# Performance work log

Measured on AMD Instinct MI355X. Metric: run time of the kernel, lower is better.

Reference implementation:

```python
import jax, jax.numpy as jnp
import numpy as np

N_NODES = 16384
N_EDGES = 524288
N_GRAPHS = 256
IN_CH = 128
H_CH = 128   # per-head channels
HEADS = 2
LAYER_DIM = HEADS * H_CH  # 256, concat=True
POOL_DIM = 3 * LAYER_DIM  # 768
OUT_CH = 1
NEG_SLOPE = 0.2


def setup_inputs() -> dict:
    key = jax.random.key(0)
    ks = jax.random.split(key, 20)
    s = lambda k, shape, fan: jax.random.normal(k, shape, jnp.float32) * (1.0 / np.sqrt(fan))
    inp = {
        "x": jax.random.normal(ks[0], (N_NODES, IN_CH), jnp.float32),
        "edge_index": jax.random.randint(ks[1], (2, N_EDGES), 0, N_NODES, jnp.int64),
        "batch": jnp.sort(jax.random.randint(ks[2], (N_NODES,), 0, N_GRAPHS, jnp.int64)),
        # GATv2 layer 1 (in=128)
        "Wl1": s(ks[3], (IN_CH, LAYER_DIM), IN_CH), "Wr1": s(ks[4], (IN_CH, LAYER_DIM), IN_CH),
        "att1": s(ks[5], (HEADS, H_CH), H_CH), "b1": jnp.zeros((LAYER_DIM,), jnp.float32),
        # GATv2 layer 2 (in=256)
        "Wl2": s(ks[6], (LAYER_DIM, LAYER_DIM), LAYER_DIM), "Wr2": s(ks[7], (LAYER_DIM, LAYER_DIM), LAYER_DIM),
        "att2": s(ks[8], (HEADS, H_CH), H_CH), "b2": jnp.zeros((LAYER_DIM,), jnp.float32),
        # GATv2 layer 3 (in=256)
        "Wl3": s(ks[9], (LAYER_DIM, LAYER_DIM), LAYER_DIM), "Wr3": s(ks[10], (LAYER_DIM, LAYER_DIM), LAYER_DIM),
        "att3": s(ks[11], (HEADS, H_CH), H_CH), "b3": jnp.zeros((LAYER_DIM,), jnp.float32),
        # FFN (dropout inactive at eval)
        "fW1": s(ks[12], (POOL_DIM, POOL_DIM), POOL_DIM), "fb1": jnp.zeros((POOL_DIM,), jnp.float32),
        "fW2": s(ks[13], (POOL_DIM, OUT_CH), POOL_DIM), "fb2": jnp.zeros((OUT_CH,), jnp.float32),
    }
    return inp


def _gatv2(x, src, dst, Wl, Wr, att, b):
    """PyG GATv2Conv: per-edge score a . LeakyReLU(Wl x_src + Wr x_dst),
    softmax over incoming edges per destination, weighted scatter-add of Wl x_src."""
    n = x.shape[0]
    xl = (x @ Wl).reshape(n, HEADS, H_CH)  # source messages
    xr = (x @ Wr).reshape(n, HEADS, H_CH)  # target query
    e = jax.nn.leaky_relu(xl[src] + xr[dst], NEG_SLOPE)          # [E,H,C]
    logits = jnp.einsum('ehc,hc->eh', e, att)                    # [E,H]
    m = jax.ops.segment_max(logits, dst, num_segments=n)         # per-dst max (self-loops guarantee nonempty)
    ev = jnp.exp(logits - m[dst])
    denom = jax.ops.segment_sum(ev, dst, num_segments=n)
    alpha = ev / denom[dst]                                       # [E,H]
    out = jax.ops.segment_sum(alpha[..., None] * xl[src], dst, num_segments=n)  # [N,H,C]
    return out.reshape(n, LAYER_DIM) + b


def reference(x, edge_index, batch, Wl1, Wr1, att1, b1, Wl2, Wr2, att2, b2,
              Wl3, Wr3, att3, b3, fW1, fb1, fW2, fb2):
    n = x.shape[0]
    loops = jnp.arange(n, dtype=edge_index.dtype)
    src = jnp.concatenate([edge_index[0], loops])  # add_self_loops=True default
    dst = jnp.concatenate([edge_index[1], loops])
    h1 = _gatv2(x, src, dst, Wl1, Wr1, att1, b1)
    h2 = _gatv2(h1, src, dst, Wl2, Wr2, att2, b2)
    h3 = _gatv2(h2, src, dst, Wl3, Wr3, att3, b3)
    pool = lambda h: jax.ops.segment_sum(h, batch, num_segments=N_GRAPHS)
    h = jnp.concatenate([pool(h1), pool(h2), pool(h3)], axis=1)   # [G,768]
    h = jax.nn.relu(h @ fW1 + fb1)
    return h @ fW2 + fb2                                           # [G,1]
```

## Files before the change

### kernel.cpp

```cpp
#include <hip/hip_runtime.h>

#define NNODES 16384
#define NEDGES 524288
#define NETOT  (NEDGES + NNODES)
#define NGRAPH 256

typedef __attribute__((ext_vector_type(8))) short short8;
typedef __attribute__((ext_vector_type(4))) float f32x4;
typedef __attribute__((ext_vector_type(2))) float f32x2;
typedef __attribute__((ext_vector_type(4))) unsigned int u32x4;

__device__ __forceinline__ float b2f(unsigned short u){
  union { unsigned int i; float f; } v; v.i = ((unsigned int)u) << 16; return v.f;
}
__device__ __forceinline__ unsigned short f2b(float f){
  union { float f; unsigned int i; } v; v.f = f;
  unsigned int r = v.i + 0x7FFFu + ((v.i >> 16) & 1u);
  return (unsigned short)(r >> 16);
}
__device__ __forceinline__ f32x2 unpack2(unsigned int u){
  union { unsigned int i; float f; } lo, hi;
  lo.i = u << 16; hi.i = u & 0xFFFF0000u;
  f32x2 r; r[0] = lo.f; r[1] = hi.f; return r;
}

__global__ void __launch_bounds__(256) zero_deg(int* __restrict__ deg){
  deg[blockIdx.x * 256 + threadIdx.x] = 0;
}

__global__ void __launch_bounds__(256) count_deg(const int* __restrict__ ei, int* __restrict__ deg){
  int i = blockIdx.x * 256 + threadIdx.x;
  int d = (i < NEDGES) ? ei[NEDGES + i] : (i - NEDGES);
  atomicAdd(&deg[d], 1);
}

__global__ void __launch_bounds__(256) scan1(const int* __restrict__ deg,
                                             int* __restrict__ incl, int* __restrict__ bsum){
  __shared__ int ws[4];
  const int b = blockIdx.x, t = threadIdx.x, lane = t & 63, w = t >> 6;
  int v = deg[b * 256 + t];
  int x = v;
  #pragma unroll
  for(int o = 1; o < 64; o <<= 1){ int u = __shfl_up(x, o, 64); if(lane >= o) x += u; }
  if(lane == 63) ws[w] = x;
  __syncthreads();
  int add = 0;
  #pragma unroll
  for(int j = 0; j < 4; j++) if(j < w) add += ws[j];
  incl[b * 256 + t] = x + add;
  if(t == 255) bsum[b] = x + add;
}

__global__ void __launch_bounds__(256) scan3(const int* __restrict__ deg, const int* __restrict__ incl,
                                             const int* __restrict__ bsum,
                                             int* __restrict__ row_off, int* __restrict__ cursor){
  __shared__ int boff_s;
  const int b = blockIdx.x, t = threadIdx.x;
  if(t < 64){
    int v = (t < b) ? bsum[t] : 0;
    #pragma unroll
    for(int o = 32; o > 0; o >>= 1) v += __shfl_xor(v, o, 64);
    if(t == 0) boff_s = v;
  }
  __syncthreads();
  const int i = b * 256 + t;
  int inc = incl[i] + boff_s;
  row_off[i + 1] = inc;
  cursor[i] = inc - deg[i];
  if(i == 0) row_off[0] = 0;
}

__global__ void __launch_bounds__(256) fill_csr(const int* __restrict__ ei, int* __restrict__ cursor,
                                                int* __restrict__ col_src){
  int i = blockIdx.x * 256 + threadIdx.x;
  int s, d;
  if(i < NEDGES){ s = ei[i]; d = ei[NEDGES + i]; }
  else          { s = i - NEDGES; d = s; }
  int p = atomicAdd(&cursor[d], 1);
  col_src[p] = s;
}

__global__ void __launch_bounds__(256) prep(const float* __restrict__ x,
                                            const float* __restrict__ Wl1, const float* __restrict__ Wr1,
                                            const float* __restrict__ Wl2, const float* __restrict__ Wr2,
                                            const float* __restrict__ Wl3, const float* __restrict__ Wr3,
                                            unsigned short* __restrict__ xb,
                                            unsigned short* __restrict__ Wt1,
                                            unsigned short* __restrict__ Wt2,
                                            unsigned short* __restrict__ Wt3){
  const int b = blockIdx.x, t = threadIdx.x;
  if(b < 8192){
    int i = b * 256 + t;
    xb[i] = f2b(x[i]);
    return;
  }
  const float *Wl, *Wr; unsigned short* Wt; int K, i;
  if(b < 8192 + 256){ Wl = Wl1; Wr = Wr1; Wt = Wt1; K = 128; i = (b - 8192) * 256 + t; }
  else if(b < 8192 + 256 + 512){ Wl = Wl2; Wr = Wr2; Wt = Wt2; K = 256; i = (b - 8448) * 256 + t; }
  else { Wl = Wl3; Wr = Wr3; Wt = Wt3; K = 256; i = (b - 8960) * 256 + t; }
  int k = i >> 9, c = i & 511;
  float val = (c < 256) ? Wl[(size_t)k * 256 + c] : Wr[(size_t)k * 256 + (c - 256)];
  Wt[(size_t)c * K + k] = f2b(val);
}

template<int K>
__global__ void __launch_bounds__(256) gemm_xw(const unsigned short* __restrict__ A,
                                               const unsigned short* __restrict__ Wt,
                                               unsigned short* __restrict__ Cout){
  __shared__ unsigned short As[64][40];
  __shared__ unsigned short Bs[128][40];
  const int t = threadIdx.x;
  const int rowbase = blockIdx.x * 64;
  const int colbase = blockIdx.y * 128;
  const int wave = t >> 6, lane = t & 63;
  const int lrow = lane & 15, kg = lane >> 4;

  f32x4 acc[8] = {};

  for(int kt = 0; kt < K; kt += 32){
    {
      int oct = t & 3, r = t >> 2;
      *(short8*)(&As[r][oct * 8]) =
        *(const short8*)(A + (size_t)(rowbase + r) * K + kt + oct * 8);
    }
    {
      int n = t & 127, kh = (t >> 7) * 16;
      const unsigned short* gw = Wt + (size_t)(colbase + n) * K + kt + kh;
      short8 v0 = *(const short8*)gw;
      short8 v1 = *(const short8*)(gw + 8);
      *(short8*)(&Bs[n][kh])     = v0;
      *(short8*)(&Bs[n][kh + 8]) = v1;
    }
    __syncthreads();
    short8 afrag = *(const short8*)(&As[wave * 16 + lrow][kg * 8]);
    #pragma unroll
    for(int fc = 0; fc < 8; fc++){
      short8 bfrag = *(const short8*)(&Bs[fc * 16 + lrow][kg * 8]);
      acc[fc] = __builtin_amdgcn_mfma_f32_16x16x32_bf16(afrag, bfrag, acc[fc], 0, 0, 0);
    }
    __syncthreads();
  }
  #pragma unroll
  for(int fc = 0; fc < 8; fc++)
    #pragma unroll
    for(int r = 0; r < 4; r++){
      int row = rowbase + wave * 16 + kg * 4 + r;
      int col = colbase + fc * 16 + lrow;
      Cout[(size_t)row * 512 + col] = f2b(acc[fc][r]);
    }
}

__global__ void __launch_bounds__(256) edge_agg(const unsigned short* __restrict__ xlb,
                                                const int* __restrict__ row_off,
                                                const int* __restrict__ col_src,
                                                const float* __restrict__ att,
                                                const float* __restrict__ bias,
                                                unsigned short* __restrict__ hout){
  const int n = (blockIdx.x * 256 + threadIdx.x) >> 6;
  const int lane = threadIdx.x & 63;
  const int eg = lane >> 4;
  const int c0 = (lane & 15) * 16;
  f32x2 xr[8], at[8];
  {
    const unsigned short* xp = xlb + (size_t)n * 512 + 256 + c0;
    u32x4 v0 = *(const u32x4*)xp;
    u32x4 v1 = *(const u32x4*)(xp + 8);
    xr[0] = unpack2(v0.x); xr[1] = unpack2(v0.y); xr[2] = unpack2(v0.z); xr[3] = unpack2(v0.w);
    xr[4] = unpack2(v1.x); xr[5] = unpack2(v1.y); xr[6] = unpack2(v1.z); xr[7] = unpack2(v1.w);
    #pragma unroll
    for(int i = 0; i < 8; i++) at[i] = *(const f32x2*)(att + c0 + 2 * i);
  }
  float s = 0.f;
  f32x2 ac[8] = {};
  const int beg = row_off[n], end = row_off[n + 1];
  for(int ch = beg; ch < end; ch += 64){
    int idx = ch + lane;
    int si = (idx < end) ? col_src[idx] : 0;
    int cnt = end - ch; if(cnt > 64) cnt = 64;
    int src0 = __shfl(si, eg);
    const unsigned short* gp0 = xlb + (size_t)src0 * 512 + c0;
    u32x4 va = *(const u32x4*)gp0;
    u32x4 vb = *(const u32x4*)(gp0 + 8);
    for(int k = 0; k < cnt; k += 4){
      int nk = k + 4 + eg; nk = (nk > 63) ? 63 : nk;
      int nsrc = __shfl(si, nk);
      const unsigned short* gpn = xlb + (size_t)nsrc * 512 + c0;
      u32x4 na = *(const u32x4*)gpn;
      u32x4 nb = *(const u32x4*)(gpn + 8);
      f32x2 x0 = unpack2(va.x), x1 = unpack2(va.y), x2 = unpack2(va.z), x3 = unpack2(va.w);
      f32x2 x4 = unpack2(vb.x), x5 = unpack2(vb.y), x6 = unpack2(vb.z), x7 = unpack2(vb.w);
      f32x2 e, p2;
      e = x0 + xr[0]; e = __builtin_elementwise_max(e, e * 0.2f); p2  = e * at[0];
      e = x1 + xr[1]; e = __builtin_elementwise_max(e, e * 0.2f); p2 += e * at[1];
      e = x2 + xr[2]; e = __builtin_elementwise_max(e, e * 0.2f); p2 += e * at[2];
      e = x3 + xr[3]; e = __builtin_elementwise_max(e, e * 0.2f); p2 += e * at[3];
      e = x4 + xr[4]; e = __builtin_elementwise_max(e, e * 0.2f); p2 += e * at[4];
      e = x5 + xr[5]; e = __builtin_elementwise_max(e, e * 0.2f); p2 += e * at[5];
      e = x6 + xr[6]; e = __builtin_elementwise_max(e, e * 0.2f); p2 += e * at[6];
      e = x7 + xr[7]; e = __builtin_elementwise_max(e, e * 0.2f); p2 += e * at[7];
      float p = p2[0] + p2[1];
      p += __shfl_xor(p, 1); p += __shfl_xor(p, 2); p += __shfl_xor(p, 4);
      float pe = (k + eg < cnt) ? __expf(p) : 0.f;
      s += pe;
      f32x2 pe2 = {pe, pe};
      ac[0] += pe2 * x0; ac[1] += pe2 * x1; ac[2] += pe2 * x2; ac[3] += pe2 * x3;
      ac[4] += pe2 * x4; ac[5] += pe2 * x5; ac[6] += pe2 * x6; ac[7] += pe2 * x7;
      va = na; vb = nb;
    }
  }
  s += __shfl_xor(s, 16); s += __shfl_xor(s, 32);
  #pragma unroll
  for(int i = 0; i < 8; i++){
    ac[i][0] += __shfl_xor(ac[i][0], 16); ac[i][0] += __shfl_xor(ac[i][0], 32);
    ac[i][1] += __shfl_xor(ac[i][1], 16); ac[i][1] += __shfl_xor(ac[i][1], 32);
  }
  if(eg == 0){
    float inv = 1.f / s;
    unsigned short o[16];
    #pragma unroll
    for(int i = 0; i < 8; i++){
      o[2 * i]     = f2b(fmaf(ac[i][0], inv, bias[c0 + 2 * i]));
      o[2 * i + 1] = f2b(fmaf(ac[i][1], inv, bias[c0 + 2 * i + 1]));
    }
    unsigned short* hp = hout + (size_t)n * 256 + c0;
    *(u32x4*)hp       = *(const u32x4*)&o[0];
    *(u32x4*)(hp + 8) = *(const u32x4*)&o[8];
  }
}

__device__ __forceinline__ int lbound(const int* __restrict__ a, int n, int v){
  int lo = 0, hi = n;
  while(lo < hi){ int mid = (lo + hi) >> 1; if(a[mid] < v) lo = mid + 1; else hi = mid; }
  return lo;
}

__global__ void __launch_bounds__(256) pool_accum(const unsigned short* __restrict__ h,
                                                  const int* __restrict__ batch,
                                                  float* __restrict__ pool, int slot){
  __shared__ float red[8][264];
  const int g = blockIdx.x, t = threadIdx.x;
  const int ng = t >> 5, c0 = (t & 31) * 8;
  const int lo = lbound(batch, NNODES, g);
  const int hi = lbound(batch, NNODES, g + 1);
  f32x2 a0 = {0.f,0.f}, a1 = {0.f,0.f}, a2 = {0.f,0.f}, a3 = {0.f,0.f};
  for(int node = lo + ng; node < hi; node += 8){
    u32x4 v = *(const u32x4*)(h + (size_t)node * 256 + c0);
    a0 += unpack2(v.x); a1 += unpack2(v.y); a2 += unpack2(v.z); a3 += unpack2(v.w);
  }
  red[ng][c0 + 0] = a0[0]; red[ng][c0 + 1] = a0[1];
  red[ng][c0 + 2] = a1[0]; red[ng][c0 + 3] = a1[1];
  red[ng][c0 + 4] = a2[0]; red[ng][c0 + 5] = a2[1];
  red[ng][c0 + 6] = a3[0]; red[ng][c0 + 7] = a3[1];
  __syncthreads();
  float s = 0.f;
  #pragma unroll
  for(int i = 0; i < 8; i++) s += red[i][t];
  pool[(size_t)g * 768 + slot * 256 + t] = s;
}

__global__ void __launch_bounds__(256) ffn1(const float* __restrict__ pool,
                                            const float* __restrict__ fW1,
                                            const float* __restrict__ fb1,
                                            float* __restrict__ hidden){
  __shared__ float ap[32][65];
  __shared__ float ws[64][33];
  const int t = threadIdx.x;
  const int cb = blockIdx.x * 32;
  const int gb = blockIdx.y * 32;
  const int tc = t & 31, tg = t >> 5;
  float acc[4] = {};
  for(int kc = 0; kc < 768; kc += 64){
    {
      int g_l = t >> 3, j8 = (t & 7) * 8;
      const float* gp = pool + (size_t)(gb + g_l) * 768 + kc + j8;
      #pragma unroll
      for(int i = 0; i < 8; i++) ap[g_l][j8 + i] = gp[i];
    }
    {
      int c_l = t & 31, k0 = (t >> 5) * 8;
      #pragma unroll
      for(int i = 0; i < 8; i++) ws[k0 + i][c_l] = fW1[(size_t)(kc + k0 + i) * 768 + cb + c_l];
    }
    __syncthreads();
    #pragma unroll
    for(int k = 0; k < 64; k++){
      float w = ws[k][tc];
      #pragma unroll
      for(int i = 0; i < 4; i++) acc[i] = fmaf(ap[tg * 4 + i][k], w, acc[i]);
    }
    __syncthreads();
  }
  float b = fb1[cb + tc];
  #pragma unroll
  for(int i = 0; i < 4; i++)
    hidden[(size_t)(gb + tg * 4 + i) * 768 + cb + tc] = fmaxf(acc[i] + b, 0.f);
}

__global__ void __launch_bounds__(256) ffn2(const float* __restrict__ hidden,
                                            const float* __restrict__ fW2,
                                            const float* __restrict__ fb2,
                                            float* __restrict__ out){
  const int g = (blockIdx.x * 256 + threadIdx.x) >> 6;
  const int lane = threadIdx.x & 63;
  float p = 0.f;
  for(int i = lane; i < 768; i += 64) p += hidden[(size_t)g * 768 + i] * fW2[i];
  #pragma unroll
  for(int o = 32; o > 0; o >>= 1) p += __shfl_xor(p, o, 64);
  if(lane == 0) out[g] = p + fb2[0];
}

extern "C" void kernel_launch(void* const* d_in, const int* in_sizes, int n_in,
                              void* d_out, int out_size, void* d_ws, size_t ws_size,
                              hipStream_t stream){
  const float* x    = (const float*)d_in[0];
  const int* ei     = (const int*)d_in[1];
  const int* batch  = (const int*)d_in[2];
  const float* Wl[3]  = {(const float*)d_in[3],  (const float*)d_in[7],  (const float*)d_in[11]};
  const float* Wr[3]  = {(const float*)d_in[4],  (const float*)d_in[8],  (const float*)d_in[12]};
  const float* att[3] = {(const float*)d_in[5],  (const float*)d_in[9],  (const float*)d_in[13]};
  const float* bp[3]  = {(const float*)d_in[6],  (const float*)d_in[10], (const float*)d_in[14]};
  const float* fW1 = (const float*)d_in[15];
  const float* fb1 = (const float*)d_in[16];
  const float* fW2 = (const float*)d_in[17];
  const float* fb2 = (const float*)d_in[18];

  char* ws = (char*)d_ws;
  size_t off = 0;
  auto alloc = [&](size_t sz){ size_t p = off; off += (sz + 255) & ~(size_t)255; return p; };
  int* deg      = (int*)(ws + alloc((size_t)NNODES * 4));
  int* rowoff   = (int*)(ws + alloc((size_t)(NNODES + 1) * 4));
  int* cursor   = (int*)(ws + alloc((size_t)NNODES * 4));
  int* colsrc   = (int*)(ws + alloc((size_t)NETOT * 4));
  int* incl     = (int*)(ws + alloc((size_t)NNODES * 4));
  int* bsum     = (int*)(ws + alloc(64 * 4));
  unsigned short* xb  = (unsigned short*)(ws + alloc((size_t)NNODES * 128 * 2));
  unsigned short* Wt1 = (unsigned short*)(ws + alloc((size_t)512 * 128 * 2));
  unsigned short* Wt2 = (unsigned short*)(ws + alloc((size_t)512 * 256 * 2));
  unsigned short* Wt3 = (unsigned short*)(ws + alloc((size_t)512 * 256 * 2));
  unsigned short* xlb = (unsigned short*)(ws + alloc((size_t)NNODES * 512 * 2));
  unsigned short* hA  = (unsigned short*)(ws + alloc((size_t)NNODES * 256 * 2));
  unsigned short* hB  = (unsigned short*)(ws + alloc((size_t)NNODES * 256 * 2));
  float* pool   = (float*)(ws + alloc((size_t)NGRAPH * 768 * 4));
  float* hidden = (float*)(ws + alloc((size_t)NGRAPH * 768 * 4));

  zero_deg<<<NNODES / 256, 256, 0, stream>>>(deg);
  count_deg<<<NETOT / 256, 256, 0, stream>>>(ei, deg);
  prep<<<8192 + 256 + 512 + 512, 256, 0, stream>>>(x, Wl[0], Wr[0], Wl[1], Wr[1], Wl[2], Wr[2],
                                                   xb, Wt1, Wt2, Wt3);
  scan1<<<NNODES / 256, 256, 0, stream>>>(deg, incl, bsum);
  scan3<<<NNODES / 256, 256, 0, stream>>>(deg, incl, bsum, rowoff, cursor);
  fill_csr<<<NETOT / 256, 256, 0, stream>>>(ei, cursor, colsrc);

  dim3 ggrid(NNODES / 64, 4);
  const int EAG = NNODES / 4;

  unsigned short* hbuf[3] = {hA, hB, hA};
  const unsigned short* abuf[3] = {xb, hA, hB};
  unsigned short* wbuf[3] = {Wt1, Wt2, Wt3};

  for(int L = 0; L < 3; L++){
    if(L == 0) gemm_xw<128><<<ggrid, 256, 0, stream>>>(abuf[0], wbuf[0], xlb);
    else       gemm_xw<256><<<ggrid, 256, 0, stream>>>(abuf[L], wbuf[L], xlb);
    edge_agg<<<EAG, 256, 0, stream>>>(xlb, rowoff, colsrc, att[L], bp[L], hbuf[L]);
    pool_accum<<<NGRAPH, 256, 0, stream>>>(hbuf[L], batch, pool, L);
  }

  ffn1<<<dim3(768 / 32, NGRAPH / 32), 256, 0, stream>>>(pool, fW1, fb1, hidden);
  ffn2<<<NGRAPH / 4, 256, 0, stream>>>(hidden, fW2, fb2, (float*)d_out);
}
```

Measured before the change: 291.4 us.

## Enlarge GEMM tile to 128 rows, use direct global-to-LDS loads with XOR swizzle

The node-feature GEMM now computes a 128x128 tile per block, with each wave owning 32 rows (two MFMA row fragments), so each B fragment is reused twice. Tiles are staged with global_load_lds straight into LDS instead of going through registers, and an XOR swizzle replaces the padded layout to avoid bank conflicts. This halves the grid size and raises accumulator register use. The GEMMs are a small part of the total next to edge aggregation.

```diff
diff --git a/kernel.cpp b/kernel.cpp
--- a/kernel.cpp
+++ b/kernel.cpp
@@ -107,47 +107,65 @@
 __global__ void __launch_bounds__(256) gemm_xw(const unsigned short* __restrict__ A,
                                                const unsigned short* __restrict__ Wt,
                                                unsigned short* __restrict__ Cout){
-  __shared__ unsigned short As[64][40];
-  __shared__ unsigned short Bs[128][40];
+  __shared__ unsigned short As[128 * 32];
+  __shared__ unsigned short Bs[128 * 32];
   const int t = threadIdx.x;
-  const int rowbase = blockIdx.x * 64;
+  const int rowbase = blockIdx.x * 128;
   const int colbase = blockIdx.y * 128;
   const int wave = t >> 6, lane = t & 63;
   const int lrow = lane & 15, kg = lane >> 4;
 
-  f32x4 acc[8] = {};
+  f32x4 acc[2][8] = {};
 
   for(int kt = 0; kt < K; kt += 32){
-    {
-      int oct = t & 3, r = t >> 2;
-      *(short8*)(&As[r][oct * 8]) =
-        *(const short8*)(A + (size_t)(rowbase + r) * K + kt + oct * 8);
-    }
-    {
-      int n = t & 127, kh = (t >> 7) * 16;
-      const unsigned short* gw = Wt + (size_t)(colbase + n) * K + kt + kh;
-      short8 v0 = *(const short8*)gw;
-      short8 v1 = *(const short8*)(gw + 8);
-      *(short8*)(&Bs[n][kh])     = v0;
-      *(short8*)(&Bs[n][kh + 8]) = v1;
+    #pragma unroll
+    for(int j = 0; j < 2; j++){
+      const int ci  = (j * 4 + wave) * 64 + lane;
+      const int row = ci >> 2, cst = ci & 3;
+      const int c   = cst ^ ((row >> 1) & 3);
+      const unsigned short* ga = A  + (size_t)(rowbase + row) * K + kt + c * 8;
+      const unsigned short* gb = Wt + (size_t)(colbase + row) * K + kt + c * 8;
+      __builtin_amdgcn_global_load_lds(
+        (const __attribute__((address_space(1))) unsigned int*)ga,
+        (__attribute__((address_space(3))) unsigned int*)(As + (j * 4 + wave) * 512),
+        16, 0, 0);
+      __builtin_amdgcn_global_load_lds(
+        (const __attribute__((address_space(1))) unsigned int*)gb,
+        (__attribute__((address_space(3))) unsigned int*)(Bs + (j * 4 + wave) * 512),
+        16, 0, 0);
     }
     __syncthreads();
-    short8 afrag = *(const short8*)(&As[wave * 16 + lrow][kg * 8]);
+
+    short8 afrag[2], bfrag[8];
+    #pragma unroll
+    for(int rf = 0; rf < 2; rf++){
+      int ra = wave * 32 + rf * 16 + lrow;
+      int ca = kg ^ ((ra >> 1) & 3);
+      afrag[rf] = *(const short8*)(As + ra * 32 + ca * 8);
+    }
     #pragma unroll
     for(int fc = 0; fc < 8; fc++){
-      short8 bfrag = *(const short8*)(&Bs[fc * 16 + lrow][kg * 8]);
-      acc[fc] = __builtin_amdgcn_mfma_f32_16x16x32_bf16(afrag, bfrag, acc[fc], 0, 0, 0);
-    }
+      int rb = fc * 16 + lrow;
+      int cb = kg ^ ((rb >> 1) & 3);
+      bfrag[fc] = *(const short8*)(Bs + rb * 32 + cb * 8);
+    }
+    #pragma unroll
+    for(int rf = 0; rf < 2; rf++)
+      #pragma unroll
+      for(int fc = 0; fc < 8; fc++)
+        acc[rf][fc] = __builtin_amdgcn_mfma_f32_16x16x32_bf16(afrag[rf], bfrag[fc], acc[rf][fc], 0, 0, 0);
     __syncthreads();
   }
   #pragma unroll
-  for(int fc = 0; fc < 8; fc++)
-    #pragma unroll
-    for(int r = 0; r < 4; r++){
-      int row = rowbase + wave * 16 + kg * 4 + r;
-      int col = colbase + fc * 16 + lrow;
-      Cout[(size_t)row * 512 + col] = f2b(acc[fc][r]);
-    }
+  for(int rf = 0; rf < 2; rf++)
+    #pragma unroll
+    for(int fc = 0; fc < 8; fc++)
+      #pragma unroll
+      for(int r = 0; r < 4; r++){
+        int row = rowbase + wave * 32 + rf * 16 + kg * 4 + r;
+        int col = colbase + fc * 16 + lrow;
+        Cout[(size_t)row * 512 + col] = f2b(acc[rf][fc][r]);
+      }
 }
 
 __global__ void __launch_bounds__(256) edge_agg(const unsigned short* __restrict__ xlb,
@@ -351,7 +369,7 @@
   scan3<<<NNODES / 256, 256, 0, stream>>>(deg, incl, bsum, rowoff, cursor);
   fill_csr<<<NETOT / 256, 256, 0, stream>>>(ei, cursor, colsrc);
 
-  dim3 ggrid(NNODES / 64, 4);
+  dim3 ggrid(NNODES / 128, 4);
   const int EAG = NNODES / 4;
 
   unsigned short* hbuf[3] = {hA, hB, hA};
```

New measurement: 277.4 us. -4.8%, faster.
